# Performance work log

Hardware: AMD Instinct MI355X
Metric: run time of the kernel (lower is better)

## Reference

```python
import jax, jax.numpy as jnp
import numpy as np
import math

KV_STRIDE = 2
Q_STRIDE = 1
WAVE_LEN = 1000.0
POS_MAG = 1.0


def _pos_embed(h, w, h_kv, w_kv, q_stride, kv_stride, feat_dim):
    # Sinusoidal relative-position embeddings, matching get_position_embedding.
    h_idx = jnp.arange(h, dtype=jnp.float32) * q_stride
    w_idx = jnp.arange(w, dtype=jnp.float32) * q_stride
    h_kv_idx = jnp.arange(h_kv, dtype=jnp.float32) * kv_stride
    w_kv_idx = jnp.arange(w_kv, dtype=jnp.float32) * kv_stride
    h_diff = (h_idx[:, None] - h_kv_idx[None, :]) * POS_MAG  # (h, h_kv)
    w_diff = (w_idx[:, None] - w_kv_idx[None, :]) * POS_MAG  # (w, w_kv)
    feat_range = jnp.arange(feat_dim // 4, dtype=jnp.float32)
    dim_mat = WAVE_LEN ** (4.0 / feat_dim * feat_range)  # (feat_dim//4,)
    wd = w_diff[:, :, None] / dim_mat  # (w, w_kv, F)
    hd = h_diff[:, :, None] / dim_mat  # (h, h_kv, F)
    emb_x = jnp.concatenate([jnp.sin(wd), jnp.cos(wd)], axis=2)  # (w, w_kv, feat_dim//2)
    emb_y = jnp.concatenate([jnp.sin(hd), jnp.cos(hd)], axis=2)  # (h, h_kv, feat_dim//2)
    return emb_x, emb_y


def setup_inputs() -> dict:
    key = jax.random.key(0)
    ks = jax.random.split(key, 11)
    C = 288
    s = 1.0 / math.sqrt(C)
    return {
        'x_input': jax.random.normal(ks[0], (2, C, 64, 64), jnp.float32),
        'Wq': jax.random.normal(ks[1], (C, C), jnp.float32) * s,
        'Wk': jax.random.normal(ks[2], (C, C), jnp.float32) * s,
        'Wv': jax.random.normal(ks[3], (C, C), jnp.float32) * s,
        'Wx': jax.random.normal(ks[4], (C, C // 2), jnp.float32) * s,
        'Wy': jax.random.normal(ks[5], (C, C // 2), jnp.float32) * s,
        'Wproj': jax.random.normal(ks[6], (C, C), jnp.float32) * s,
        'bproj': jax.random.normal(ks[7], (C,), jnp.float32) * 0.02,
        'Wc': jax.random.normal(ks[8], (9, C), jnp.float32) * s,
        'bc': jax.random.normal(ks[9], (9,), jnp.float32) * 0.02,
        'gamma': jax.random.normal(ks[10], (1,), jnp.float32),
    }


def reference(x_input, Wq, Wk, Wv, Wx, Wy, Wproj, bproj, Wc, bc, gamma):
    M = Wc.shape[0]                       # num_mixtures
    n, C, h, w = x_input.shape
    d = Wq.shape[0] // M                  # qk_embed_dim (== v_dim)
    x_q = x_input                         # q_stride == 1
    x_kv = x_input[:, :, ::KV_STRIDE, ::KV_STRIDE]  # AvgPool2d(k=1, stride=2)
    h_kv, w_kv = x_kv.shape[2], x_kv.shape[3]

    # 1x1 convs as channel GEMMs
    q = jnp.einsum('nchw,oc->nohw', x_q, Wq).reshape(n, M, d, h * w)
    q = q.transpose(0, 1, 3, 2)                                    # (n,M,hw,d)
    k = jnp.einsum('nchw,oc->nohw', x_kv, Wk).reshape(n, M, d, h_kv * w_kv)

    emb_x, emb_y = _pos_embed(h, w, h_kv, w_kv, Q_STRIDE, KV_STRIDE, C)
    inv_sqrt2 = 1.0 / math.sqrt(2.0)
    pf_x = (emb_x @ Wx.T).reshape(w, w_kv, M, d).transpose(2, 0, 1, 3) * inv_sqrt2  # (M,w,w_kv,d)
    pf_y = (emb_y @ Wy.T).reshape(h, h_kv, M, d).transpose(2, 0, 1, 3) * inv_sqrt2  # (M,h,h_kv,d)

    energy = jnp.matmul(q, k).reshape(n, M, h, w, h_kv, w_kv)
    q5 = q.reshape(n, M, h, w, d)
    e_x = jnp.einsum('nmhwd,mwvd->nmhwv', q5, pf_x)  # (n,M,h,w,w_kv)
    e_y = jnp.einsum('nmhwd,mhud->nmhwu', q5, pf_y)  # (n,M,h,w,h_kv)
    energy = energy + e_x[:, :, :, :, None, :] + e_y[:, :, :, :, :, None]
    energy = energy.reshape(n, M, h * w, h_kv * w_kv)
    attn = jax.nn.softmax(energy, axis=3)

    # Learned per-mixture gating from mean query context
    context = q.transpose(0, 1, 3, 2).reshape(n, M * d, h * w).mean(axis=2)  # (n, M*d)
    mix_w = jax.nn.softmax(context @ Wc.T + bc, axis=1)                      # (n, M)
    attn = jnp.sum(attn * mix_w[:, :, None, None], axis=1)                   # (n,hw,hw_kv)

    v = jnp.einsum('nchw,oc->nohw', x_kv, Wv).reshape(n, M * d, h_kv * w_kv)
    v = v.transpose(0, 2, 1)                                                 # (n,hw_kv,M*d)
    out = jnp.matmul(attn, v).transpose(0, 2, 1).reshape(n, M * d, h, w)
    out = jnp.einsum('nchw,oc->nohw', out, Wproj) + bproj[None, :, None, None]
    return gamma[0] * out + x_input
```

## Files before the change

kernel.cpp:

```cpp
#include <hip/hip_runtime.h>
#include <math.h>

#define NB     2
#define CDIM   288
#define HW     4096
#define PKV    1024
#define MHEAD  9
#define DHEAD  32

typedef __attribute__((ext_vector_type(8))) short bf16x8;
typedef __attribute__((ext_vector_type(4))) float f32x4;

__device__ inline unsigned short f2bf(float x) {
    unsigned int u = __float_as_uint(x);
    u = (u + 0x7fffu + ((u >> 16) & 1u)) >> 16;
    return (unsigned short)u;
}


__global__ __launch_bounds__(64) void wcvtF(const float* __restrict__ A, const float* __restrict__ B,
        const float* __restrict__ C, const float* __restrict__ D,
        unsigned short* __restrict__ oA, unsigned short* __restrict__ oB,
        unsigned short* __restrict__ oC, unsigned short* __restrict__ oD) {
    int t  = blockIdx.x;
    int ot = t / 9, cc = t % 9;
    const float* W = (blockIdx.y == 0) ? A : (blockIdx.y == 1) ? B : (blockIdx.y == 2) ? C : D;
    unsigned short* O = ((blockIdx.y == 0) ? oA : (blockIdx.y == 1) ? oB : (blockIdx.y == 2) ? oC : oD)
                        + (size_t)t * 512;
    int lane = threadIdx.x;
    int o  = ot * 16 + (lane & 15);
    int c0 = cc * 32 + (lane >> 4) * 8;
    const float* src = W + (size_t)o * CDIM + c0;
    float4 f0 = *(const float4*)src, f1 = *(const float4*)(src + 4);
    unsigned int v0 = f2bf(f0.x) | ((unsigned int)f2bf(f0.y) << 16);
    unsigned int v1 = f2bf(f0.z) | ((unsigned int)f2bf(f0.w) << 16);
    unsigned int v2 = f2bf(f1.x) | ((unsigned int)f2bf(f1.y) << 16);
    unsigned int v3 = f2bf(f1.z) | ((unsigned int)f2bf(f1.w) << 16);
    uint4 pk = { v0, v1, v2, v3 };
    *(uint4*)(O + lane * 8) = pk;
}

__global__ __launch_bounds__(256) void xtransF(const float* __restrict__ X,
                                               unsigned short* __restrict__ XF) {
    int n = blockIdx.z, j0 = blockIdx.x * 32, c0 = blockIdx.y * 32;
    __shared__ float t[32][33];
    int tx = threadIdx.x & 31, ty = threadIdx.x >> 5;
#pragma unroll
    for (int l = 0; l < 4; ++l) {
        int c = ty + l * 8;
        t[c][tx] = X[((size_t)n * CDIM + c0 + c) * HW + j0 + tx];
    }
    __syncthreads();
    int s = threadIdx.x >> 7;
    int u = threadIdx.x & 127;
    int lane = u >> 1, e0 = (u & 1) * 4;
    int jl = s * 16 + (lane & 15);
    int cb = (lane >> 4) * 8 + e0;
    unsigned int w0 = f2bf(t[cb + 0][jl]) | ((unsigned int)f2bf(t[cb + 1][jl]) << 16);
    unsigned int w1 = f2bf(t[cb + 2][jl]) | ((unsigned int)f2bf(t[cb + 3][jl]) << 16);
    int jt = (j0 >> 4) + s, cc = c0 >> 5;
    unsigned short* O = XF + (size_t)n * HW * CDIM + ((size_t)jt * 9 + cc) * 512 + lane * 8 + e0;
    uint2 pk = { w0, w1 };
    *(uint2*)O = pk;
}

__global__ __launch_bounds__(256) void gemm_q_F(const unsigned short* __restrict__ WF,
        const unsigned short* __restrict__ XF, unsigned short* __restrict__ Qf) {
    int n  = blockIdx.z;
    int m  = blockIdx.y;
    int j0 = blockIdx.x * 128;
    int wv = threadIdx.x >> 6, lane = threadIdx.x & 63;
    int jw = j0 + wv * 32;
    const unsigned short* Wb = WF + ((size_t)(m * 2) * 9) * 512 + lane * 8;
    const unsigned short* Xb = XF + (size_t)n * HW * CDIM + ((size_t)(jw >> 4) * 9) * 512 + lane * 8;
    f32x4 acc[2][2] = {};
#pragma unroll
    for (int cc = 0; cc < 9; ++cc) {
        bf16x8 a0 = *(const bf16x8*)(Wb + (size_t)cc * 512);
        bf16x8 a1 = *(const bf16x8*)(Wb + (size_t)(9 + cc) * 512);
        bf16x8 b0 = *(const bf16x8*)(Xb + (size_t)cc * 512);
        bf16x8 b1 = *(const bf16x8*)(Xb + (size_t)(9 + cc) * 512);
        acc[0][0] = __builtin_amdgcn_mfma_f32_16x16x32_bf16(a0, b0, acc[0][0], 0, 0, 0);
        acc[0][1] = __builtin_amdgcn_mfma_f32_16x16x32_bf16(a0, b1, acc[0][1], 0, 0, 0);
        acc[1][0] = __builtin_amdgcn_mfma_f32_16x16x32_bf16(a1, b0, acc[1][0], 0, 0, 0);
        acc[1][1] = __builtin_amdgcn_mfma_f32_16x16x32_bf16(a1, b1, acc[1][1], 0, 0, 0);
    }
    __shared__ __attribute__((aligned(16))) unsigned short trq[4][32][40];
    int lq = lane & 15, quad = lane >> 4;
#pragma unroll
    for (int oi = 0; oi < 2; ++oi)
#pragma unroll
        for (int ji = 0; ji < 2; ++ji)
#pragma unroll
            for (int r = 0; r < 4; ++r)
                trq[wv][ji * 16 + lq][oi * 16 + quad * 4 + r] = f2bf(acc[oi][ji][r]);
    int jl = lane & 31, half = lane >> 5;
    bf16x8 v0 = *(const bf16x8*)&trq[wv][jl][half * 16];
    bf16x8 v1 = *(const bf16x8*)&trq[wv][jl][half * 16 + 8];
    unsigned short* Qm = Qf + ((size_t)(n * MHEAD + m) * HW + jw + jl) * 32 + half * 16;
    *(bf16x8*)Qm = v0;
    *(bf16x8*)(Qm + 8) = v1;
}

__global__ __launch_bounds__(256) void gemm_kv_F(const unsigned short* __restrict__ WkF,
        const unsigned short* __restrict__ WvF, const unsigned short* __restrict__ XF,
        unsigned short* __restrict__ KF, unsigned short* __restrict__ VF) {
    int n  = blockIdx.z;
    int m  = blockIdx.y;
    int p0 = blockIdx.x * 128;
    int wv = threadIdx.x >> 6, lane = threadIdx.x & 63;
    int pw = p0 + wv * 32;
    int lq = lane & 15, quad = lane >> 4;
    const unsigned short* XFn = XF + (size_t)n * HW * CDIM;
    size_t bidx[2];
#pragma unroll
    for (int pi = 0; pi < 2; ++pi) {
        int p   = pw + pi * 16 + lq;
        int pos = ((p >> 5) << 7) + ((p & 31) << 1);
        bidx[pi] = ((size_t)(pos >> 4) * 9) * 512 + ((pos & 15) + 16 * quad) * 8;
    }
    const unsigned short* Wkb = WkF + ((size_t)(m * 2) * 9) * 512 + lane * 8;
    const unsigned short* Wvb = WvF + ((size_t)(m * 2) * 9) * 512 + lane * 8;
    f32x4 ak[2][2] = {}, av[2][2] = {};
#pragma unroll
    for (int cc = 0; cc < 9; ++cc) {
        bf16x8 a0k = *(const bf16x8*)(Wkb + (size_t)cc * 512);
        bf16x8 a1k = *(const bf16x8*)(Wkb + (size_t)(9 + cc) * 512);
        bf16x8 a0v = *(const bf16x8*)(Wvb + (size_t)cc * 512);
        bf16x8 a1v = *(const bf16x8*)(Wvb + (size_t)(9 + cc) * 512);
        bf16x8 b0  = *(const bf16x8*)(XFn + bidx[0] + (size_t)cc * 512);
        bf16x8 b1  = *(const bf16x8*)(XFn + bidx[1] + (size_t)cc * 512);
        ak[0][0] = __builtin_amdgcn_mfma_f32_16x16x32_bf16(a0k, b0, ak[0][0], 0, 0, 0);
        ak[0][1] = __builtin_amdgcn_mfma_f32_16x16x32_bf16(a0k, b1, ak[0][1], 0, 0, 0);
        ak[1][0] = __builtin_amdgcn_mfma_f32_16x16x32_bf16(a1k, b0, ak[1][0], 0, 0, 0);
        ak[1][1] = __builtin_amdgcn_mfma_f32_16x16x32_bf16(a1k, b1, ak[1][1], 0, 0, 0);
        av[0][0] = __builtin_amdgcn_mfma_f32_16x16x32_bf16(a0v, b0, av[0][0], 0, 0, 0);
        av[0][1] = __builtin_amdgcn_mfma_f32_16x16x32_bf16(a0v, b1, av[0][1], 0, 0, 0);
        av[1][0] = __builtin_amdgcn_mfma_f32_16x16x32_bf16(a1v, b0, av[1][0], 0, 0, 0);
        av[1][1] = __builtin_amdgcn_mfma_f32_16x16x32_bf16(a1v, b1, av[1][1], 0, 0, 0);
    }
    __shared__ __attribute__((aligned(16))) unsigned short tr[4][32][40];
#pragma unroll
    for (int oi = 0; oi < 2; ++oi)
#pragma unroll
        for (int pi = 0; pi < 2; ++pi)
#pragma unroll
            for (int r = 0; r < 4; ++r)
                tr[wv][pi * 16 + lq][oi * 16 + quad * 4 + r] = f2bf(ak[oi][pi][r]);
    unsigned short* KFm = KF + (size_t)(n * MHEAD + m) * (PKV * 32);
#pragma unroll
    for (int pi = 0; pi < 2; ++pi) {
        bf16x8 v = *(const bf16x8*)&tr[wv][pi * 16 + lq][quad * 8];
        *(bf16x8*)(KFm + (size_t)((pw >> 4) + pi) * 512 + lane * 8) = v;
    }
#pragma unroll
    for (int oi = 0; oi < 2; ++oi)
#pragma unroll
        for (int pi = 0; pi < 2; ++pi)
#pragma unroll
            for (int r = 0; r < 4; ++r)
                tr[wv][oi * 16 + quad * 4 + r][pi * 16 + lq] = f2bf(av[oi][pi][r]);
    unsigned short* VFn = VF + (size_t)n * CDIM * PKV;
#pragma unroll
    for (int oi = 0; oi < 2; ++oi) {
        bf16x8 v = *(const bf16x8*)&tr[wv][oi * 16 + lq][quad * 8];
        *(bf16x8*)(VFn + (size_t)((m * 2 + oi) * 32 + (pw >> 5)) * 512 + lane * 8) = v;
    }
}

__global__ __launch_bounds__(256) void gemm_av_F(const unsigned short* __restrict__ VF,
        const unsigned short* __restrict__ AF, unsigned short* __restrict__ MF) {
    int n  = blockIdx.z;
    int oc = blockIdx.y;
    int wv = threadIdx.x >> 6, lane = threadIdx.x & 63;
    int it = blockIdx.x * 4 + wv;
    const unsigned short* An = AF + (size_t)n * HW * PKV + (size_t)it * 32 * 512 + lane * 8;
    const unsigned short* Vn = VF + (size_t)n * CDIM * PKV + lane * 8;
    f32x4 acc[2] = {};
#pragma unroll 4
    for (int pc = 0; pc < 32; ++pc) {
        bf16x8 a  = *(const bf16x8*)(An + (size_t)pc * 512);
        bf16x8 b0 = *(const bf16x8*)(Vn + (size_t)((oc * 2 + 0) * 32 + pc) * 512);
        bf16x8 b1 = *(const bf16x8*)(Vn + (size_t)((oc * 2 + 1) * 32 + pc) * 512);
        acc[0] = __builtin_amdgcn_mfma_f32_16x16x32_bf16(a, b0, acc[0], 0, 0, 0);
        acc[1] = __builtin_amdgcn_mfma_f32_16x16x32_bf16(a, b1, acc[1], 0, 0, 0);
    }
    __shared__ __attribute__((aligned(16))) unsigned short trm[4][16][40];
    int lq = lane & 15, quad = lane >> 4;
#pragma unroll
    for (int oi = 0; oi < 2; ++oi)
#pragma unroll
        for (int r = 0; r < 4; ++r)
            trm[wv][quad * 4 + r][oi * 16 + lq] = f2bf(acc[oi][r]);
    bf16x8 v = *(const bf16x8*)&trm[wv][lq][quad * 8];
    unsigned short* O = MF + (size_t)n * HW * CDIM + ((size_t)it * 9 + oc) * 512 + lane * 8;
    *(bf16x8*)O = v;
}

__global__ __launch_bounds__(256) void gemm_proj_F(const unsigned short* __restrict__ WFp,
        const unsigned short* __restrict__ MF, const float* __restrict__ bproj,
        const float* __restrict__ x, const float* __restrict__ gamma,
        float* __restrict__ OUT) {
    int n  = blockIdx.z;
    int o0 = blockIdx.y * 32;
    int j0 = blockIdx.x * 128;
    int wv = threadIdx.x >> 6, lane = threadIdx.x & 63;
    int jw = j0 + wv * 32;
    const unsigned short* Wb = WFp + ((size_t)(o0 >> 4) * 9) * 512 + lane * 8;
    const unsigned short* Mb = MF + (size_t)n * HW * CDIM + ((size_t)(jw >> 4) * 9) * 512 + lane * 8;
    f32x4 acc[2][2] = {};
#pragma unroll
    for (int cc = 0; cc < 9; ++cc) {
        bf16x8 a0 = *(const bf16x8*)(Wb + (size_t)cc * 512);
        bf16x8 a1 = *(const bf16x8*)(Wb + (size_t)(9 + cc) * 512);
        bf16x8 b0 = *(const bf16x8*)(Mb + (size_t)cc * 512);
        bf16x8 b1 = *(const bf16x8*)(Mb + (size_t)(9 + cc) * 512);
        acc[0][0] = __builtin_amdgcn_mfma_f32_16x16x32_bf16(a0, b0, acc[0][0], 0, 0, 0);
        acc[0][1] = __builtin_amdgcn_mfma_f32_16x16x32_bf16(a0, b1, acc[0][1], 0, 0, 0);
        acc[1][0] = __builtin_amdgcn_mfma_f32_16x16x32_bf16(a1, b0, acc[1][0], 0, 0, 0);
        acc[1][1] = __builtin_amdgcn_mfma_f32_16x16x32_bf16(a1, b1, acc[1][1], 0, 0, 0);
    }
    float g = gamma[0];
    int lq = lane & 15, quad = lane >> 4;
#pragma unroll
    for (int oi = 0; oi < 2; ++oi)
#pragma unroll
        for (int ji = 0; ji < 2; ++ji)
#pragma unroll
            for (int r = 0; r < 4; ++r) {
                int o = o0 + oi * 16 + quad * 4 + r;
                size_t idx = ((size_t)(n * CDIM) + o) * HW + jw + ji * 16 + lq;
                OUT[idx] = g * (acc[oi][ji][r] + bproj[o]) + x[idx];
            }
}

__global__ void wtrans(const float* __restrict__ Wx, const float* __restrict__ Wy,
                       float* __restrict__ WTx, float* __restrict__ WTy) {
    __shared__ float t[16][17];
    const float* W = blockIdx.z ? Wy : Wx;
    float* WT      = blockIdx.z ? WTy : WTx;
    int f0 = blockIdx.x * 16, o0 = blockIdx.y * 16;
    int tx = threadIdx.x, ty = threadIdx.y;
    t[ty][tx] = W[(o0 + ty) * 144 + f0 + tx];
    __syncthreads();
    WT[(f0 + ty) * 288 + o0 + tx] = t[tx][ty];
}

__global__ __launch_bounds__(320) void pff_kernel(const float* __restrict__ WTx,
        const float* __restrict__ WTy, float* __restrict__ FX, float* __restrict__ FY) {
    int blk  = blockIdx.x;
    int axis = blk / 126;
    int dif  = blk % 126;
    __shared__ float emb[144];
    int tid = threadIdx.x;
    float diff = (float)(dif - 62);
    if (tid < 72) {
        float dm = expf(6.9077552789821368f * ((float)tid * (1.f / 72.f)));
        float t  = diff / dm;
        emb[tid]      = sinf(t);
        emb[72 + tid] = cosf(t);
    }
    __syncthreads();
    if (tid < 288) {
        const float* WT = axis ? WTy : WTx;
        float s = 0.f;
#pragma unroll 8
        for (int f = 0; f < 144; ++f) s += emb[f] * WT[f * 288 + tid];
        int m = tid >> 5, d = tid & 31;
        float* F = axis ? FY : FX;
        F[((size_t)m * 126 + dif) * 32 + d] = s * 0.70710678118654752f;
    }
}

__global__ __launch_bounds__(256) void exey_kernel(const unsigned short* __restrict__ Qf,
        const float* __restrict__ FX, const float* __restrict__ FY,
        float* __restrict__ EX, float* __restrict__ EY) {
    int axis = blockIdx.x >> 6;
    int g    = blockIdx.x & 63;
    int m    = blockIdx.y;
    int n    = blockIdx.z;
    int tid  = threadIdx.x;
    size_t Qbase = (size_t)(n * MHEAD + m) * HW;

    __shared__ float fS[32][36];
    __shared__ unsigned int qSu[64][20];

    {
        const float* F = axis ? FY : FX;
        int v = tid >> 3, d0 = (tid & 7) * 4;
        *(float4*)&fS[v][d0] = *(const float4*)&F[((size_t)m * 126 + g + 62 - 2 * v) * 32 + d0];
    }
#pragma unroll
    for (int l = 0; l < 4; ++l) {
        int idx = tid + l * 256;
        int r = idx >> 4, c = idx & 15;
        int i = axis ? (g * 64 + r) : (r * 64 + g);
        qSu[r][c] = *(const unsigned int*)&Qf[(Qbase + i) * 32 + 2 * c];
    }
    __syncthreads();

    int r  = tid >> 2;
    int vg = tid & 3;
    float qv[32];
#pragma unroll
    for (int k = 0; k < 4; ++k) {
        uint4 qa = *(const uint4*)&qSu[r][k * 4];
        unsigned int uu[4] = { qa.x, qa.y, qa.z, qa.w };
#pragma unroll
        for (int e = 0; e < 4; ++e) {
            qv[k * 8 + 2 * e]     = __uint_as_float(uu[e] << 16);
            qv[k * 8 + 2 * e + 1] = __uint_as_float(uu[e] & 0xffff0000u);
        }
    }
    float acc8[8] = {};
#pragma unroll
    for (int k4 = 0; k4 < 8; ++k4) {
        float qx = qv[4 * k4], qy = qv[4 * k4 + 1], qz = qv[4 * k4 + 2], qw = qv[4 * k4 + 3];
#pragma unroll
        for (int t = 0; t < 8; ++t) {
            float4 f4 = *(const float4*)&fS[vg * 8 + t][k4 * 4];
            acc8[t] += qx * f4.x + qy * f4.y + qz * f4.z + qw * f4.w;
        }
    }
    int i = axis ? (g * 64 + r) : (r * 64 + g);
    float* out = axis ? EY : EX;
    size_t obase = (Qbase + i) * 32 + vg * 8;
    float4 s0 = { acc8[0], acc8[1], acc8[2], acc8[3] };
    float4 s1 = { acc8[4], acc8[5], acc8[6], acc8[7] };
    *(float4*)&out[obase]     = s0;
    *(float4*)&out[obase + 4] = s1;
}

__global__ void meanx_kernel(const float* __restrict__ X, float* __restrict__ MX) {
    int bid = blockIdx.x;
    const float* xr = X + (size_t)bid * HW;
    int tid = threadIdx.x;
    float s = 0.f;
    for (int j = tid; j < HW; j += 256) s += xr[j];
    for (int off = 32; off > 0; off >>= 1) s += __shfl_xor(s, off, 64);
    __shared__ float red[4];
    if ((tid & 63) == 0) red[tid >> 6] = s;
    __syncthreads();
    if (tid == 0) MX[bid] = (red[0] + red[1] + red[2] + red[3]) * (1.f / 4096.f);
}

__global__ void mixw2_kernel(const float* __restrict__ Wq, const float* __restrict__ MX,
                             const float* __restrict__ Wc, const float* __restrict__ bc,
                             float* __restrict__ MIXW) {
    __shared__ float ctx_s[NB * CDIM];
    __shared__ float lg[18];
    int tid = threadIdx.x;
    for (int p = tid; p < NB * CDIM; p += 256) {
        int n = p / CDIM, o = p % CDIM;
        const float* wr = Wq + (size_t)o * CDIM;
        const float* mx = MX + n * CDIM;
        float s = 0.f;
        for (int c = 0; c < CDIM; c += 4) {
            float4 w4 = *(const float4*)&wr[c];
            float4 m4 = *(const float4*)&mx[c];
            s += w4.x * m4.x + w4.y * m4.y + w4.z * m4.z + w4.w * m4.w;
        }
        ctx_s[p] = s;
    }
    __syncthreads();
    if (tid < 18) {
        int n = tid / 9, j = tid % 9;
        float s = bc[j];
        for (int o = 0; o < CDIM; ++o) s += ctx_s[n * CDIM + o] * Wc[j * CDIM + o];
        lg[tid] = s;
    }
    __syncthreads();
    if (tid < 2) {
        float mx = -1e30f;
        for (int j = 0; j < 9; ++j) mx = fmaxf(mx, lg[tid * 9 + j]);
        float e[9], sm = 0.f;
        for (int j = 0; j < 9; ++j) { e[j] = __expf(lg[tid * 9 + j] - mx); sm += e[j]; }
        for (int j = 0; j < 9; ++j) MIXW[tid * 9 + j] = e[j] / sm;
    }
}

__global__ __launch_bounds__(512, 4) void attn_v5(
        const unsigned short* __restrict__ Qf, const unsigned short* __restrict__ KF,
        const float* __restrict__ EX, const float* __restrict__ EY,
        const float* __restrict__ MIXW, unsigned short* __restrict__ AF) {
    int n    = blockIdx.x >> 8;
    int i0   = (blockIdx.x & 255) * 16;
    int tid  = threadIdx.x;
    int wv   = tid >> 6;
    int lane = tid & 63;
    int lq   = lane & 15;
    int quad = lane >> 4;

    __shared__ float ext_s[16][33];
    __shared__ float eyt_s[16][33];
    __shared__ float ws_s[8][16];
    __shared__ float ltot_s[16];
    __shared__ __attribute__((aligned(16))) unsigned short tr[16][1032];

    float mixed[8][4];
#pragma unroll
    for (int t = 0; t < 8; ++t)
#pragma unroll
        for (int j = 0; j < 4; ++j) mixed[t][j] = 0.f;

    int sq = tid >> 5, sv = tid & 31;

    for (int m = 0; m < MHEAD; ++m) {
        const unsigned short* Qm  = Qf + ((size_t)(n * MHEAD + m) * HW + i0) * 32;
        const unsigned short* KmF = KF + (size_t)(n * MHEAD + m) * (PKV * 32);
        size_t ebase = ((size_t)(n * MHEAD + m) * HW + i0 + sq) * 32 + sv;
        __syncthreads();
        ext_s[sq][sv] = EX[ebase];
        eyt_s[sq][sv] = EY[ebase];
        __syncthreads();

        bf16x8 afrag = *(const bf16x8*)(Qm + (size_t)lq * 32 + quad * 8);
        float exA[4], exB[4];
#pragma unroll
        for (int j = 0; j < 4; ++j) {
            exA[j] = ext_s[quad * 4 + j][lq];
            exB[j] = ext_s[quad * 4 + j][16 + lq];
        }

        bf16x8 bf[8];
#pragma unroll
        for (int t = 0; t < 8; ++t)
            bf[t] = *(const bf16x8*)(KmF + (size_t)(wv * 8 + t) * 512 + lane * 8);
        f32x4 acc[8];
#pragma unroll
        for (int t = 0; t < 8; ++t) acc[t] = (f32x4){0.f, 0.f, 0.f, 0.f};
#pragma unroll
        for (int t = 0; t < 8; ++t)
            acc[t] = __builtin_amdgcn_mfma_f32_16x16x32_bf16(afrag, bf[t], acc[t], 0, 0, 0);

        float rs[4] = {0.f, 0.f, 0.f, 0.f};
#pragma unroll
        for (int t = 0; t < 8; ++t) {
            int u = wv * 4 + (t >> 1);
            bool hi = t & 1;
#pragma unroll
            for (int j = 0; j < 4; ++j) {
                float e = __expf(acc[t][j] + (hi ? exB[j] : exA[j]) + eyt_s[quad * 4 + j][u]);
                rs[j] += e;
                acc[t][j] = e;
            }
        }
#pragma unroll
        for (int j = 0; j < 4; ++j) {
            rs[j] += __shfl_xor(rs[j], 1, 64);
            rs[j] += __shfl_xor(rs[j], 2, 64);
            rs[j] += __shfl_xor(rs[j], 4, 64);
            rs[j] += __shfl_xor(rs[j], 8, 64);
        }
        if (lq == 0) {
#pragma unroll
            for (int j = 0; j < 4; ++j) ws_s[wv][quad * 4 + j] = rs[j];
        }
        __syncthreads();
        if (tid < 16) {
            float s = 0.f;
#pragma unroll
            for (int w = 0; w < 8; ++w) s += ws_s[w][tid];
            ltot_s[tid] = s;
        }
        __syncthreads();

        float wm = MIXW[n * MHEAD + m];
        float fct[4];
#pragma unroll
        for (int j = 0; j < 4; ++j) fct[j] = wm / ltot_s[quad * 4 + j];
#pragma unroll
        for (int t = 0; t < 8; ++t)
#pragma unroll
            for (int j = 0; j < 4; ++j) mixed[t][j] += acc[t][j] * fct[j];
    }

#pragma unroll
    for (int t = 0; t < 8; ++t)
#pragma unroll
        for (int j = 0; j < 4; ++j)
            tr[quad * 4 + j][wv * 128 + t * 16 + lq] = f2bf(mixed[t][j]);
    __syncthreads();
    unsigned short* AFn = AF + (size_t)n * HW * PKV + (size_t)(i0 >> 4) * 32 * 512;
#pragma unroll
    for (int pc2 = 0; pc2 < 4; ++pc2) {
        int pc = wv * 4 + pc2;
        bf16x8 v = *(const bf16x8*)&tr[lane & 15][pc * 32 + (lane >> 4) * 8];
        *(bf16x8*)(AFn + (size_t)pc * 512 + lane * 8) = v;
    }
}

extern "C" void kernel_launch(void* const* d_in, const int* in_sizes, int n_in,
                              void* d_out, int out_size, void* d_ws, size_t ws_size,
                              hipStream_t stream) {
    const float* x     = (const float*)d_in[0];
    const float* Wq    = (const float*)d_in[1];
    const float* Wk    = (const float*)d_in[2];
    const float* Wv    = (const float*)d_in[3];
    const float* Wx    = (const float*)d_in[4];
    const float* Wy    = (const float*)d_in[5];
    const float* Wproj = (const float*)d_in[6];
    const float* bproj = (const float*)d_in[7];
    const float* Wc    = (const float*)d_in[8];
    const float* bc    = (const float*)d_in[9];
    const float* gamma = (const float*)d_in[10];
    float* out = (float*)d_out;

    float* ws = (float*)d_ws;
    size_t off = 0;
    unsigned short* Qf  = (unsigned short*)(ws + off); off += (size_t)NB * MHEAD * HW * 32 / 2;
    unsigned short* KF  = (unsigned short*)(ws + off); off += (size_t)NB * MHEAD * PKV * 32 / 2;
    unsigned short* VF  = (unsigned short*)(ws + off); off += (size_t)NB * CDIM * PKV / 2;
    unsigned short* WFq = (unsigned short*)(ws + off); off += (size_t)CDIM * CDIM / 2;
    unsigned short* WFk = (unsigned short*)(ws + off); off += (size_t)CDIM * CDIM / 2;
    unsigned short* WFv = (unsigned short*)(ws + off); off += (size_t)CDIM * CDIM / 2;
    unsigned short* WFp = (unsigned short*)(ws + off); off += (size_t)CDIM * CDIM / 2;
    unsigned short* XF  = (unsigned short*)(ws + off); off += (size_t)NB * HW * CDIM / 2;
    float* WTx  = ws + off; off += 144 * 288;
    float* WTy  = ws + off; off += 144 * 288;
    float* FX   = ws + off; off += (size_t)MHEAD * 126 * 32;
    float* FY   = ws + off; off += (size_t)MHEAD * 126 * 32;
    float* EX   = ws + off; off += (size_t)NB * MHEAD * HW * 32;
    float* EY   = ws + off; off += (size_t)NB * MHEAD * HW * 32;
    float* MX   = ws + off; off += NB * CDIM;
    float* MIXW = ws + off; off += 32;
    unsigned short* AF = (unsigned short*)(ws + off); off += (size_t)NB * HW * PKV / 2;
    unsigned short* MF = (unsigned short*)(ws + off); off += (size_t)NB * HW * CDIM / 2;

    wcvtF<<<dim3(162, 4), 64, 0, stream>>>(Wq, Wk, Wv, Wproj, WFq, WFk, WFv, WFp);
    xtransF<<<dim3(HW / 32, CDIM / 32, NB), 256, 0, stream>>>(x, XF);
    wtrans<<<dim3(9, 18, 2), dim3(16, 16), 0, stream>>>(Wx, Wy, WTx, WTy);
    pff_kernel<<<252, 320, 0, stream>>>(WTx, WTy, FX, FY);
    gemm_q_F<<<dim3(HW / 128, CDIM / 32, NB), 256, 0, stream>>>(WFq, XF, Qf);
    gemm_kv_F<<<dim3(PKV / 128, CDIM / 32, NB), 256, 0, stream>>>(WFk, WFv, XF, KF, VF);
    meanx_kernel<<<NB * CDIM, 256, 0, stream>>>(x, MX);
    mixw2_kernel<<<1, 256, 0, stream>>>(Wq, MX, Wc, bc, MIXW);
    exey_kernel<<<dim3(128, MHEAD, NB), 256, 0, stream>>>(Qf, FX, FY, EX, EY);
    attn_v5<<<NB * HW / 16, 512, 0, stream>>>(Qf, KF, EX, EY, MIXW, AF);
    gemm_av_F<<<dim3(HW / 64, CDIM / 32, NB), 256, 0, stream>>>(VF, AF, MF);
    gemm_proj_F<<<dim3(HW / 128, CDIM / 32, NB), 256, 0, stream>>>(WFp, MF, bproj, x, gamma, out);
}
```

Baseline: 212.6 us.

## Fuse attention with PV and projection GEMMs, merge prep and QKV kernels

The attention kernel now multiplies its mixed probability tile by V and then by the projection weights directly from shared memory, writing the final residual output. This removes the bf16 attention matrix AF and the intermediate MF round trips through global memory, along with two launches. The weight conversion, x transpose, Wx/Wy transpose and mean reduction kernels are merged into one prep kernel, and the Q and KV GEMMs into one launch, cutting launch overhead. In exchange each attention block does more serial work, uses more shared memory, and rereads V and Wproj from global/L2 per 16-row tile.

```diff
diff --git a/kernel.cpp b/kernel.cpp
--- a/kernel.cpp
+++ b/kernel.cpp
@@ -18,232 +18,176 @@
 }
 
 
-__global__ __launch_bounds__(64) void wcvtF(const float* __restrict__ A, const float* __restrict__ B,
-        const float* __restrict__ C, const float* __restrict__ D,
-        unsigned short* __restrict__ oA, unsigned short* __restrict__ oB,
-        unsigned short* __restrict__ oC, unsigned short* __restrict__ oD) {
-    int t  = blockIdx.x;
-    int ot = t / 9, cc = t % 9;
-    const float* W = (blockIdx.y == 0) ? A : (blockIdx.y == 1) ? B : (blockIdx.y == 2) ? C : D;
-    unsigned short* O = ((blockIdx.y == 0) ? oA : (blockIdx.y == 1) ? oB : (blockIdx.y == 2) ? oC : oD)
-                        + (size_t)t * 512;
-    int lane = threadIdx.x;
-    int o  = ot * 16 + (lane & 15);
-    int c0 = cc * 32 + (lane >> 4) * 8;
-    const float* src = W + (size_t)o * CDIM + c0;
-    float4 f0 = *(const float4*)src, f1 = *(const float4*)(src + 4);
-    unsigned int v0 = f2bf(f0.x) | ((unsigned int)f2bf(f0.y) << 16);
-    unsigned int v1 = f2bf(f0.z) | ((unsigned int)f2bf(f0.w) << 16);
-    unsigned int v2 = f2bf(f1.x) | ((unsigned int)f2bf(f1.y) << 16);
-    unsigned int v3 = f2bf(f1.z) | ((unsigned int)f2bf(f1.w) << 16);
-    uint4 pk = { v0, v1, v2, v3 };
-    *(uint4*)(O + lane * 8) = pk;
-}
-
-__global__ __launch_bounds__(256) void xtransF(const float* __restrict__ X,
-                                               unsigned short* __restrict__ XF) {
-    int n = blockIdx.z, j0 = blockIdx.x * 32, c0 = blockIdx.y * 32;
-    __shared__ float t[32][33];
-    int tx = threadIdx.x & 31, ty = threadIdx.x >> 5;
-#pragma unroll
-    for (int l = 0; l < 4; ++l) {
-        int c = ty + l * 8;
-        t[c][tx] = X[((size_t)n * CDIM + c0 + c) * HW + j0 + tx];
-    }
-    __syncthreads();
-    int s = threadIdx.x >> 7;
-    int u = threadIdx.x & 127;
-    int lane = u >> 1, e0 = (u & 1) * 4;
-    int jl = s * 16 + (lane & 15);
-    int cb = (lane >> 4) * 8 + e0;
-    unsigned int w0 = f2bf(t[cb + 0][jl]) | ((unsigned int)f2bf(t[cb + 1][jl]) << 16);
-    unsigned int w1 = f2bf(t[cb + 2][jl]) | ((unsigned int)f2bf(t[cb + 3][jl]) << 16);
-    int jt = (j0 >> 4) + s, cc = c0 >> 5;
-    unsigned short* O = XF + (size_t)n * HW * CDIM + ((size_t)jt * 9 + cc) * 512 + lane * 8 + e0;
-    uint2 pk = { w0, w1 };
-    *(uint2*)O = pk;
-}
-
-__global__ __launch_bounds__(256) void gemm_q_F(const unsigned short* __restrict__ WF,
-        const unsigned short* __restrict__ XF, unsigned short* __restrict__ Qf) {
+__global__ __launch_bounds__(256) void prep(const float* __restrict__ X,
+        const float* __restrict__ Wq, const float* __restrict__ Wk,
+        const float* __restrict__ Wv, const float* __restrict__ Wproj,
+        const float* __restrict__ Wx, const float* __restrict__ Wy,
+        unsigned short* __restrict__ XF, unsigned short* __restrict__ WFq,
+        unsigned short* __restrict__ WFk, unsigned short* __restrict__ WFv,
+        unsigned short* __restrict__ WFp, float* __restrict__ WTx,
+        float* __restrict__ WTy, float* __restrict__ MX) {
+    __shared__ float t32[32][33];
+    __shared__ float t16[16][17];
+    __shared__ float red[4];
+    int b = blockIdx.x;
+    int tid = threadIdx.x;
+    if (b < 2304) {
+        int bx = b % 128, by = (b / 128) % 9, n = b / 1152;
+        int j0 = bx * 32, c0 = by * 32;
+        int tx = tid & 31, ty = tid >> 5;
+#pragma unroll
+        for (int l = 0; l < 4; ++l) {
+            int c = ty + l * 8;
+            t32[c][tx] = X[((size_t)n * CDIM + c0 + c) * HW + j0 + tx];
+        }
+        __syncthreads();
+        int s = tid >> 7;
+        int u = tid & 127;
+        int lane = u >> 1, e0 = (u & 1) * 4;
+        int jl = s * 16 + (lane & 15);
+        int cb = (lane >> 4) * 8 + e0;
+        unsigned int w0 = f2bf(t32[cb + 0][jl]) | ((unsigned int)f2bf(t32[cb + 1][jl]) << 16);
+        unsigned int w1 = f2bf(t32[cb + 2][jl]) | ((unsigned int)f2bf(t32[cb + 3][jl]) << 16);
+        int jt = (j0 >> 4) + s, cc = c0 >> 5;
+        unsigned short* O = XF + (size_t)n * HW * CDIM + ((size_t)jt * 9 + cc) * 512 + lane * 8 + e0;
+        uint2 pk = { w0, w1 };
+        *(uint2*)O = pk;
+    } else if (b < 2628) {
+        int u = b - 2304;
+        int bx = u % 9, by = (u / 9) % 18, bz = u / 162;
+        const float* W = bz ? Wy : Wx;
+        float* WT      = bz ? WTy : WTx;
+        int f0 = bx * 16, o0 = by * 16;
+        int tx = tid & 15, ty = tid >> 4;
+        t16[ty][tx] = W[(o0 + ty) * 144 + f0 + tx];
+        __syncthreads();
+        WT[(f0 + ty) * 288 + o0 + tx] = t16[tx][ty];
+    } else if (b < 2790) {
+        int t = b - 2628;
+        int sub = tid >> 6, lane = tid & 63;
+        int ot = t / 9, cc = t % 9;
+        const float* W = (sub == 0) ? Wq : (sub == 1) ? Wk : (sub == 2) ? Wv : Wproj;
+        unsigned short* O = ((sub == 0) ? WFq : (sub == 1) ? WFk : (sub == 2) ? WFv : WFp)
+                            + (size_t)t * 512;
+        int o  = ot * 16 + (lane & 15);
+        int c0 = cc * 32 + (lane >> 4) * 8;
+        const float* src = W + (size_t)o * CDIM + c0;
+        float4 f0 = *(const float4*)src, f1 = *(const float4*)(src + 4);
+        unsigned int v0 = f2bf(f0.x) | ((unsigned int)f2bf(f0.y) << 16);
+        unsigned int v1 = f2bf(f0.z) | ((unsigned int)f2bf(f0.w) << 16);
+        unsigned int v2 = f2bf(f1.x) | ((unsigned int)f2bf(f1.y) << 16);
+        unsigned int v3 = f2bf(f1.z) | ((unsigned int)f2bf(f1.w) << 16);
+        uint4 pk = { v0, v1, v2, v3 };
+        *(uint4*)(O + lane * 8) = pk;
+    } else {
+        int bid = b - 2790;
+        const float* xr = X + (size_t)bid * HW;
+        float s = 0.f;
+        for (int j = tid; j < HW; j += 256) s += xr[j];
+        for (int off = 32; off > 0; off >>= 1) s += __shfl_xor(s, off, 64);
+        if ((tid & 63) == 0) red[tid >> 6] = s;
+        __syncthreads();
+        if (tid == 0) MX[bid] = (red[0] + red[1] + red[2] + red[3]) * (1.f / 4096.f);
+    }
+}
+
+__global__ __launch_bounds__(256) void qkv_F(const unsigned short* __restrict__ WFq,
+        const unsigned short* __restrict__ WFk, const unsigned short* __restrict__ WFv,
+        const unsigned short* __restrict__ XF, unsigned short* __restrict__ Qf,
+        unsigned short* __restrict__ KF, unsigned short* __restrict__ VF) {
+    __shared__ __attribute__((aligned(16))) unsigned short tr[4][32][40];
     int n  = blockIdx.z;
     int m  = blockIdx.y;
-    int j0 = blockIdx.x * 128;
     int wv = threadIdx.x >> 6, lane = threadIdx.x & 63;
-    int jw = j0 + wv * 32;
-    const unsigned short* Wb = WF + ((size_t)(m * 2) * 9) * 512 + lane * 8;
-    const unsigned short* Xb = XF + (size_t)n * HW * CDIM + ((size_t)(jw >> 4) * 9) * 512 + lane * 8;
-    f32x4 acc[2][2] = {};
-#pragma unroll
-    for (int cc = 0; cc < 9; ++cc) {
-        bf16x8 a0 = *(const bf16x8*)(Wb + (size_t)cc * 512);
-        bf16x8 a1 = *(const bf16x8*)(Wb + (size_t)(9 + cc) * 512);
-        bf16x8 b0 = *(const bf16x8*)(Xb + (size_t)cc * 512);
-        bf16x8 b1 = *(const bf16x8*)(Xb + (size_t)(9 + cc) * 512);
-        acc[0][0] = __builtin_amdgcn_mfma_f32_16x16x32_bf16(a0, b0, acc[0][0], 0, 0, 0);
-        acc[0][1] = __builtin_amdgcn_mfma_f32_16x16x32_bf16(a0, b1, acc[0][1], 0, 0, 0);
-        acc[1][0] = __builtin_amdgcn_mfma_f32_16x16x32_bf16(a1, b0, acc[1][0], 0, 0, 0);
-        acc[1][1] = __builtin_amdgcn_mfma_f32_16x16x32_bf16(a1, b1, acc[1][1], 0, 0, 0);
-    }
-    __shared__ __attribute__((aligned(16))) unsigned short trq[4][32][40];
     int lq = lane & 15, quad = lane >> 4;
-#pragma unroll
-    for (int oi = 0; oi < 2; ++oi)
-#pragma unroll
-        for (int ji = 0; ji < 2; ++ji)
-#pragma unroll
-            for (int r = 0; r < 4; ++r)
-                trq[wv][ji * 16 + lq][oi * 16 + quad * 4 + r] = f2bf(acc[oi][ji][r]);
-    int jl = lane & 31, half = lane >> 5;
-    bf16x8 v0 = *(const bf16x8*)&trq[wv][jl][half * 16];
-    bf16x8 v1 = *(const bf16x8*)&trq[wv][jl][half * 16 + 8];
-    unsigned short* Qm = Qf + ((size_t)(n * MHEAD + m) * HW + jw + jl) * 32 + half * 16;
-    *(bf16x8*)Qm = v0;
-    *(bf16x8*)(Qm + 8) = v1;
-}
-
-__global__ __launch_bounds__(256) void gemm_kv_F(const unsigned short* __restrict__ WkF,
-        const unsigned short* __restrict__ WvF, const unsigned short* __restrict__ XF,
-        unsigned short* __restrict__ KF, unsigned short* __restrict__ VF) {
-    int n  = blockIdx.z;
-    int m  = blockIdx.y;
-    int p0 = blockIdx.x * 128;
-    int wv = threadIdx.x >> 6, lane = threadIdx.x & 63;
-    int pw = p0 + wv * 32;
-    int lq = lane & 15, quad = lane >> 4;
-    const unsigned short* XFn = XF + (size_t)n * HW * CDIM;
-    size_t bidx[2];
-#pragma unroll
-    for (int pi = 0; pi < 2; ++pi) {
-        int p   = pw + pi * 16 + lq;
-        int pos = ((p >> 5) << 7) + ((p & 31) << 1);
-        bidx[pi] = ((size_t)(pos >> 4) * 9) * 512 + ((pos & 15) + 16 * quad) * 8;
-    }
-    const unsigned short* Wkb = WkF + ((size_t)(m * 2) * 9) * 512 + lane * 8;
-    const unsigned short* Wvb = WvF + ((size_t)(m * 2) * 9) * 512 + lane * 8;
-    f32x4 ak[2][2] = {}, av[2][2] = {};
-#pragma unroll
-    for (int cc = 0; cc < 9; ++cc) {
-        bf16x8 a0k = *(const bf16x8*)(Wkb + (size_t)cc * 512);
-        bf16x8 a1k = *(const bf16x8*)(Wkb + (size_t)(9 + cc) * 512);
-        bf16x8 a0v = *(const bf16x8*)(Wvb + (size_t)cc * 512);
-        bf16x8 a1v = *(const bf16x8*)(Wvb + (size_t)(9 + cc) * 512);
-        bf16x8 b0  = *(const bf16x8*)(XFn + bidx[0] + (size_t)cc * 512);
-        bf16x8 b1  = *(const bf16x8*)(XFn + bidx[1] + (size_t)cc * 512);
-        ak[0][0] = __builtin_amdgcn_mfma_f32_16x16x32_bf16(a0k, b0, ak[0][0], 0, 0, 0);
-        ak[0][1] = __builtin_amdgcn_mfma_f32_16x16x32_bf16(a0k, b1, ak[0][1], 0, 0, 0);
-        ak[1][0] = __builtin_amdgcn_mfma_f32_16x16x32_bf16(a1k, b0, ak[1][0], 0, 0, 0);
-        ak[1][1] = __builtin_amdgcn_mfma_f32_16x16x32_bf16(a1k, b1, ak[1][1], 0, 0, 0);
-        av[0][0] = __builtin_amdgcn_mfma_f32_16x16x32_bf16(a0v, b0, av[0][0], 0, 0, 0);
-        av[0][1] = __builtin_amdgcn_mfma_f32_16x16x32_bf16(a0v, b1, av[0][1], 0, 0, 0);
-        av[1][0] = __builtin_amdgcn_mfma_f32_16x16x32_bf16(a1v, b0, av[1][0], 0, 0, 0);
-        av[1][1] = __builtin_amdgcn_mfma_f32_16x16x32_bf16(a1v, b1, av[1][1], 0, 0, 0);
-    }
-    __shared__ __attribute__((aligned(16))) unsigned short tr[4][32][40];
-#pragma unroll
-    for (int oi = 0; oi < 2; ++oi)
-#pragma unroll
-        for (int pi = 0; pi < 2; ++pi)
-#pragma unroll
-            for (int r = 0; r < 4; ++r)
-                tr[wv][pi * 16 + lq][oi * 16 + quad * 4 + r] = f2bf(ak[oi][pi][r]);
-    unsigned short* KFm = KF + (size_t)(n * MHEAD + m) * (PKV * 32);
-#pragma unroll
-    for (int pi = 0; pi < 2; ++pi) {
-        bf16x8 v = *(const bf16x8*)&tr[wv][pi * 16 + lq][quad * 8];
-        *(bf16x8*)(KFm + (size_t)((pw >> 4) + pi) * 512 + lane * 8) = v;
-    }
-#pragma unroll
-    for (int oi = 0; oi < 2; ++oi)
-#pragma unroll
-        for (int pi = 0; pi < 2; ++pi)
-#pragma unroll
-            for (int r = 0; r < 4; ++r)
-                tr[wv][oi * 16 + quad * 4 + r][pi * 16 + lq] = f2bf(av[oi][pi][r]);
-    unsigned short* VFn = VF + (size_t)n * CDIM * PKV;
-#pragma unroll
-    for (int oi = 0; oi < 2; ++oi) {
-        bf16x8 v = *(const bf16x8*)&tr[wv][oi * 16 + lq][quad * 8];
-        *(bf16x8*)(VFn + (size_t)((m * 2 + oi) * 32 + (pw >> 5)) * 512 + lane * 8) = v;
-    }
-}
-
-__global__ __launch_bounds__(256) void gemm_av_F(const unsigned short* __restrict__ VF,
-        const unsigned short* __restrict__ AF, unsigned short* __restrict__ MF) {
-    int n  = blockIdx.z;
-    int oc = blockIdx.y;
-    int wv = threadIdx.x >> 6, lane = threadIdx.x & 63;
-    int it = blockIdx.x * 4 + wv;
-    const unsigned short* An = AF + (size_t)n * HW * PKV + (size_t)it * 32 * 512 + lane * 8;
-    const unsigned short* Vn = VF + (size_t)n * CDIM * PKV + lane * 8;
-    f32x4 acc[2] = {};
-#pragma unroll 4
-    for (int pc = 0; pc < 32; ++pc) {
-        bf16x8 a  = *(const bf16x8*)(An + (size_t)pc * 512);
-        bf16x8 b0 = *(const bf16x8*)(Vn + (size_t)((oc * 2 + 0) * 32 + pc) * 512);
-        bf16x8 b1 = *(const bf16x8*)(Vn + (size_t)((oc * 2 + 1) * 32 + pc) * 512);
-        acc[0] = __builtin_amdgcn_mfma_f32_16x16x32_bf16(a, b0, acc[0], 0, 0, 0);
-        acc[1] = __builtin_amdgcn_mfma_f32_16x16x32_bf16(a, b1, acc[1], 0, 0, 0);
-    }
-    __shared__ __attribute__((aligned(16))) unsigned short trm[4][16][40];
-    int lq = lane & 15, quad = lane >> 4;
-#pragma unroll
-    for (int oi = 0; oi < 2; ++oi)
-#pragma unroll
-        for (int r = 0; r < 4; ++r)
-            trm[wv][quad * 4 + r][oi * 16 + lq] = f2bf(acc[oi][r]);
-    bf16x8 v = *(const bf16x8*)&trm[wv][lq][quad * 8];
-    unsigned short* O = MF + (size_t)n * HW * CDIM + ((size_t)it * 9 + oc) * 512 + lane * 8;
-    *(bf16x8*)O = v;
-}
-
-__global__ __launch_bounds__(256) void gemm_proj_F(const unsigned short* __restrict__ WFp,
-        const unsigned short* __restrict__ MF, const float* __restrict__ bproj,
-        const float* __restrict__ x, const float* __restrict__ gamma,
-        float* __restrict__ OUT) {
-    int n  = blockIdx.z;
-    int o0 = blockIdx.y * 32;
-    int j0 = blockIdx.x * 128;
-    int wv = threadIdx.x >> 6, lane = threadIdx.x & 63;
-    int jw = j0 + wv * 32;
-    const unsigned short* Wb = WFp + ((size_t)(o0 >> 4) * 9) * 512 + lane * 8;
-    const unsigned short* Mb = MF + (size_t)n * HW * CDIM + ((size_t)(jw >> 4) * 9) * 512 + lane * 8;
-    f32x4 acc[2][2] = {};
-#pragma unroll
-    for (int cc = 0; cc < 9; ++cc) {
-        bf16x8 a0 = *(const bf16x8*)(Wb + (size_t)cc * 512);
-        bf16x8 a1 = *(const bf16x8*)(Wb + (size_t)(9 + cc) * 512);
-        bf16x8 b0 = *(const bf16x8*)(Mb + (size_t)cc * 512);
-        bf16x8 b1 = *(const bf16x8*)(Mb + (size_t)(9 + cc) * 512);
-        acc[0][0] = __builtin_amdgcn_mfma_f32_16x16x32_bf16(a0, b0, acc[0][0], 0, 0, 0);
-        acc[0][1] = __builtin_amdgcn_mfma_f32_16x16x32_bf16(a0, b1, acc[0][1], 0, 0, 0);
-        acc[1][0] = __builtin_amdgcn_mfma_f32_16x16x32_bf16(a1, b0, acc[1][0], 0, 0, 0);
-        acc[1][1] = __builtin_amdgcn_mfma_f32_16x16x32_bf16(a1, b1, acc[1][1], 0, 0, 0);
-    }
-    float g = gamma[0];
-    int lq = lane & 15, quad = lane >> 4;
-#pragma unroll
-    for (int oi = 0; oi < 2; ++oi)
-#pragma unroll
-        for (int ji = 0; ji < 2; ++ji)
-#pragma unroll
-            for (int r = 0; r < 4; ++r) {
-                int o = o0 + oi * 16 + quad * 4 + r;
-                size_t idx = ((size_t)(n * CDIM) + o) * HW + jw + ji * 16 + lq;
-                OUT[idx] = g * (acc[oi][ji][r] + bproj[o]) + x[idx];
-            }
-}
-
-__global__ void wtrans(const float* __restrict__ Wx, const float* __restrict__ Wy,
-                       float* __restrict__ WTx, float* __restrict__ WTy) {
-    __shared__ float t[16][17];
-    const float* W = blockIdx.z ? Wy : Wx;
-    float* WT      = blockIdx.z ? WTy : WTx;
-    int f0 = blockIdx.x * 16, o0 = blockIdx.y * 16;
-    int tx = threadIdx.x, ty = threadIdx.y;
-    t[ty][tx] = W[(o0 + ty) * 144 + f0 + tx];
-    __syncthreads();
-    WT[(f0 + ty) * 288 + o0 + tx] = t[tx][ty];
+    if (blockIdx.x < 32) {
+        int j0 = blockIdx.x * 128;
+        int jw = j0 + wv * 32;
+        const unsigned short* Wb = WFq + ((size_t)(m * 2) * 9) * 512 + lane * 8;
+        const unsigned short* Xb = XF + (size_t)n * HW * CDIM + ((size_t)(jw >> 4) * 9) * 512 + lane * 8;
+        f32x4 acc[2][2] = {};
+#pragma unroll
+        for (int cc = 0; cc < 9; ++cc) {
+            bf16x8 a0 = *(const bf16x8*)(Wb + (size_t)cc * 512);
+            bf16x8 a1 = *(const bf16x8*)(Wb + (size_t)(9 + cc) * 512);
+            bf16x8 b0 = *(const bf16x8*)(Xb + (size_t)cc * 512);
+            bf16x8 b1 = *(const bf16x8*)(Xb + (size_t)(9 + cc) * 512);
+            acc[0][0] = __builtin_amdgcn_mfma_f32_16x16x32_bf16(a0, b0, acc[0][0], 0, 0, 0);
+            acc[0][1] = __builtin_amdgcn_mfma_f32_16x16x32_bf16(a0, b1, acc[0][1], 0, 0, 0);
+            acc[1][0] = __builtin_amdgcn_mfma_f32_16x16x32_bf16(a1, b0, acc[1][0], 0, 0, 0);
+            acc[1][1] = __builtin_amdgcn_mfma_f32_16x16x32_bf16(a1, b1, acc[1][1], 0, 0, 0);
+        }
+#pragma unroll
+        for (int oi = 0; oi < 2; ++oi)
+#pragma unroll
+            for (int ji = 0; ji < 2; ++ji)
+#pragma unroll
+                for (int r = 0; r < 4; ++r)
+                    tr[wv][ji * 16 + lq][oi * 16 + quad * 4 + r] = f2bf(acc[oi][ji][r]);
+        int jl = lane & 31, half = lane >> 5;
+        bf16x8 v0 = *(const bf16x8*)&tr[wv][jl][half * 16];
+        bf16x8 v1 = *(const bf16x8*)&tr[wv][jl][half * 16 + 8];
+        unsigned short* Qm = Qf + ((size_t)(n * MHEAD + m) * HW + jw + jl) * 32 + half * 16;
+        *(bf16x8*)Qm = v0;
+        *(bf16x8*)(Qm + 8) = v1;
+    } else {
+        int p0 = (blockIdx.x - 32) * 128;
+        int pw = p0 + wv * 32;
+        const unsigned short* XFn = XF + (size_t)n * HW * CDIM;
+        size_t bidx[2];
+#pragma unroll
+        for (int pi = 0; pi < 2; ++pi) {
+            int p   = pw + pi * 16 + lq;
+            int pos = ((p >> 5) << 7) + ((p & 31) << 1);
+            bidx[pi] = ((size_t)(pos >> 4) * 9) * 512 + ((pos & 15) + 16 * quad) * 8;
+        }
+        const unsigned short* Wkb = WFk + ((size_t)(m * 2) * 9) * 512 + lane * 8;
+        const unsigned short* Wvb = WFv + ((size_t)(m * 2) * 9) * 512 + lane * 8;
+        f32x4 ak[2][2] = {}, av[2][2] = {};
+#pragma unroll
+        for (int cc = 0; cc < 9; ++cc) {
+            bf16x8 a0k = *(const bf16x8*)(Wkb + (size_t)cc * 512);
+            bf16x8 a1k = *(const bf16x8*)(Wkb + (size_t)(9 + cc) * 512);
+            bf16x8 a0v = *(const bf16x8*)(Wvb + (size_t)cc * 512);
+            bf16x8 a1v = *(const bf16x8*)(Wvb + (size_t)(9 + cc) * 512);
+            bf16x8 b0  = *(const bf16x8*)(XFn + bidx[0] + (size_t)cc * 512);
+            bf16x8 b1  = *(const bf16x8*)(XFn + bidx[1] + (size_t)cc * 512);
+            ak[0][0] = __builtin_amdgcn_mfma_f32_16x16x32_bf16(a0k, b0, ak[0][0], 0, 0, 0);
+            ak[0][1] = __builtin_amdgcn_mfma_f32_16x16x32_bf16(a0k, b1, ak[0][1], 0, 0, 0);
+            ak[1][0] = __builtin_amdgcn_mfma_f32_16x16x32_bf16(a1k, b0, ak[1][0], 0, 0, 0);
+            ak[1][1] = __builtin_amdgcn_mfma_f32_16x16x32_bf16(a1k, b1, ak[1][1], 0, 0, 0);
+            av[0][0] = __builtin_amdgcn_mfma_f32_16x16x32_bf16(a0v, b0, av[0][0], 0, 0, 0);
+            av[0][1] = __builtin_amdgcn_mfma_f32_16x16x32_bf16(a0v, b1, av[0][1], 0, 0, 0);
+            av[1][0] = __builtin_amdgcn_mfma_f32_16x16x32_bf16(a1v, b0, av[1][0], 0, 0, 0);
+            av[1][1] = __builtin_amdgcn_mfma_f32_16x16x32_bf16(a1v, b1, av[1][1], 0, 0, 0);
+        }
+#pragma unroll
+        for (int oi = 0; oi < 2; ++oi)
+#pragma unroll
+            for (int pi = 0; pi < 2; ++pi)
+#pragma unroll
+                for (int r = 0; r < 4; ++r)
+                    tr[wv][pi * 16 + lq][oi * 16 + quad * 4 + r] = f2bf(ak[oi][pi][r]);
+        unsigned short* KFm = KF + (size_t)(n * MHEAD + m) * (PKV * 32);
+#pragma unroll
+        for (int pi = 0; pi < 2; ++pi) {
+            bf16x8 v = *(const bf16x8*)&tr[wv][pi * 16 + lq][quad * 8];
+            *(bf16x8*)(KFm + (size_t)((pw >> 4) + pi) * 512 + lane * 8) = v;
+        }
+#pragma unroll
+        for (int oi = 0; oi < 2; ++oi)
+#pragma unroll
+            for (int pi = 0; pi < 2; ++pi)
+#pragma unroll
+                for (int r = 0; r < 4; ++r)
+                    tr[wv][oi * 16 + quad * 4 + r][pi * 16 + lq] = f2bf(av[oi][pi][r]);
+        unsigned short* VFn = VF + (size_t)n * CDIM * PKV;
+#pragma unroll
+        for (int oi = 0; oi < 2; ++oi) {
+            bf16x8 v = *(const bf16x8*)&tr[wv][oi * 16 + lq][quad * 8];
+            *(bf16x8*)(VFn + (size_t)((m * 2 + oi) * 32 + (pw >> 5)) * 512 + lane * 8) = v;
+        }
+    }
 }
 
 __global__ __launch_bounds__(320) void pff_kernel(const float* __restrict__ WTx,
@@ -329,19 +273,6 @@
     float4 s1 = { acc8[4], acc8[5], acc8[6], acc8[7] };
     *(float4*)&out[obase]     = s0;
     *(float4*)&out[obase + 4] = s1;
-}
-
-__global__ void meanx_kernel(const float* __restrict__ X, float* __restrict__ MX) {
-    int bid = blockIdx.x;
-    const float* xr = X + (size_t)bid * HW;
-    int tid = threadIdx.x;
-    float s = 0.f;
-    for (int j = tid; j < HW; j += 256) s += xr[j];
-    for (int off = 32; off > 0; off >>= 1) s += __shfl_xor(s, off, 64);
-    __shared__ float red[4];
-    if ((tid & 63) == 0) red[tid >> 6] = s;
-    __syncthreads();
-    if (tid == 0) MX[bid] = (red[0] + red[1] + red[2] + red[3]) * (1.f / 4096.f);
 }
 
 __global__ void mixw2_kernel(const float* __restrict__ Wq, const float* __restrict__ MX,
@@ -379,10 +310,13 @@
     }
 }
 
-__global__ __launch_bounds__(512, 4) void attn_v5(
+__global__ __launch_bounds__(512, 4) void attn_fused(
         const unsigned short* __restrict__ Qf, const unsigned short* __restrict__ KF,
+        const unsigned short* __restrict__ VF, const unsigned short* __restrict__ WFp,
         const float* __restrict__ EX, const float* __restrict__ EY,
-        const float* __restrict__ MIXW, unsigned short* __restrict__ AF) {
+        const float* __restrict__ MIXW, const float* __restrict__ bproj,
+        const float* __restrict__ x, const float* __restrict__ gamma,
+        float* __restrict__ OUT) {
     int n    = blockIdx.x >> 8;
     int i0   = (blockIdx.x & 255) * 16;
     int tid  = threadIdx.x;
@@ -396,6 +330,7 @@
     __shared__ float ws_s[8][16];
     __shared__ float ltot_s[16];
     __shared__ __attribute__((aligned(16))) unsigned short tr[16][1032];
+    __shared__ __attribute__((aligned(16))) unsigned short Mt[16][296];
 
     float mixed[8][4];
 #pragma unroll
@@ -481,12 +416,50 @@
         for (int j = 0; j < 4; ++j)
             tr[quad * 4 + j][wv * 128 + t * 16 + lq] = f2bf(mixed[t][j]);
     __syncthreads();
-    unsigned short* AFn = AF + (size_t)n * HW * PKV + (size_t)(i0 >> 4) * 32 * 512;
-#pragma unroll
-    for (int pc2 = 0; pc2 < 4; ++pc2) {
-        int pc = wv * 4 + pc2;
-        bf16x8 v = *(const bf16x8*)&tr[lane & 15][pc * 32 + (lane >> 4) * 8];
-        *(bf16x8*)(AFn + (size_t)pc * 512 + lane * 8) = v;
+
+    const unsigned short* VFn = VF + (size_t)n * CDIM * PKV;
+    f32x4 accpv[3] = {};
+#pragma unroll 4
+    for (int pc = 0; pc < 32; ++pc) {
+        bf16x8 pf = *(const bf16x8*)&tr[lq][pc * 32 + quad * 8];
+#pragma unroll
+        for (int idx = 0; idx < 3; ++idx) {
+            int ot = wv + idx * 8;
+            if (ot < 18) {
+                bf16x8 vf = *(const bf16x8*)(VFn + (size_t)(ot * 32 + pc) * 512 + lane * 8);
+                accpv[idx] = __builtin_amdgcn_mfma_f32_16x16x32_bf16(pf, vf, accpv[idx], 0, 0, 0);
+            }
+        }
+    }
+#pragma unroll
+    for (int idx = 0; idx < 3; ++idx) {
+        int ot = wv + idx * 8;
+        if (ot < 18) {
+#pragma unroll
+            for (int r = 0; r < 4; ++r)
+                Mt[quad * 4 + r][ot * 16 + lq] = f2bf(accpv[idx][r]);
+        }
+    }
+    __syncthreads();
+
+    float g = gamma[0];
+#pragma unroll
+    for (int idx = 0; idx < 3; ++idx) {
+        int ot = wv + idx * 8;
+        if (ot >= 18) continue;
+        f32x4 acc = {};
+#pragma unroll
+        for (int cc = 0; cc < 9; ++cc) {
+            bf16x8 af = *(const bf16x8*)(WFp + (size_t)(ot * 9 + cc) * 512 + lane * 8);
+            bf16x8 bfm = *(const bf16x8*)&Mt[lq][cc * 32 + quad * 8];
+            acc = __builtin_amdgcn_mfma_f32_16x16x32_bf16(af, bfm, acc, 0, 0, 0);
+        }
+#pragma unroll
+        for (int r = 0; r < 4; ++r) {
+            int o = ot * 16 + quad * 4 + r;
+            size_t id = ((size_t)(n * CDIM) + o) * HW + i0 + lq;
+            OUT[id] = g * (acc[r] + bproj[o]) + x[id];
+        }
     }
 }
 
@@ -524,19 +497,13 @@
     float* EY   = ws + off; off += (size_t)NB * MHEAD * HW * 32;
     float* MX   = ws + off; off += NB * CDIM;
     float* MIXW = ws + off; off += 32;
-    unsigned short* AF = (unsigned short*)(ws + off); off += (size_t)NB * HW * PKV / 2;
-    unsigned short* MF = (unsigned short*)(ws + off); off += (size_t)NB * HW * CDIM / 2;
-
-    wcvtF<<<dim3(162, 4), 64, 0, stream>>>(Wq, Wk, Wv, Wproj, WFq, WFk, WFv, WFp);
-    xtransF<<<dim3(HW / 32, CDIM / 32, NB), 256, 0, stream>>>(x, XF);
-    wtrans<<<dim3(9, 18, 2), dim3(16, 16), 0, stream>>>(Wx, Wy, WTx, WTy);
+
+    prep<<<3366, 256, 0, stream>>>(x, Wq, Wk, Wv, Wproj, Wx, Wy,
+                                   XF, WFq, WFk, WFv, WFp, WTx, WTy, MX);
     pff_kernel<<<252, 320, 0, stream>>>(WTx, WTy, FX, FY);
-    gemm_q_F<<<dim3(HW / 128, CDIM / 32, NB), 256, 0, stream>>>(WFq, XF, Qf);
-    gemm_kv_F<<<dim3(PKV / 128, CDIM / 32, NB), 256, 0, stream>>>(WFk, WFv, XF, KF, VF);
-    meanx_kernel<<<NB * CDIM, 256, 0, stream>>>(x, MX);
     mixw2_kernel<<<1, 256, 0, stream>>>(Wq, MX, Wc, bc, MIXW);
+    qkv_F<<<dim3(40, MHEAD, NB), 256, 0, stream>>>(WFq, WFk, WFv, XF, Qf, KF, VF);
     exey_kernel<<<dim3(128, MHEAD, NB), 256, 0, stream>>>(Qf, FX, FY, EX, EY);
-    attn_v5<<<NB * HW / 16, 512, 0, stream>>>(Qf, KF, EX, EY, MIXW, AF);
-    gemm_av_F<<<dim3(HW / 64, CDIM / 32, NB), 256, 0, stream>>>(VF, AF, MF);
-    gemm_proj_F<<<dim3(HW / 128, CDIM / 32, NB), 256, 0, stream>>>(WFp, MF, bproj, x, gamma, out);
-}
+    attn_fused<<<NB * HW / 16, 512, 0, stream>>>(Qf, KF, VF, WFp, EX, EY, MIXW,
+                                                 bproj, x, gamma, out);
+}
```

After: 205.1 us. 1.04x faster.
